# Performance work log

Measured on AMD Instinct MI355X. Metric: run time of the kernel, lower is better.

Reference implementation:

```python
import jax, jax.numpy as jnp
import numpy as np

IM_H, IM_W = 32, 32
HEADS, HEAD_DIM = 8, 32
IN_DIM = 256
OUT_DIM = 256
N = IM_H * IM_W


def _relative_indices(h, w):
    # replicate torch meshgrid('ij') + flatten logic
    gy, gx = np.meshgrid(np.arange(h), np.arange(w), indexing='ij')
    pos = np.stack([gy.reshape(-1), gx.reshape(-1)])  # (2, n)
    rel = pos[:, :, None] - pos[:, None, :]           # (2, n, n)
    r0 = (rel[0] + (h - 1)) * (2 * w - 1)
    r1 = rel[1] + (w - 1)
    return (r0 + r1).reshape(-1)                      # (n*n,)

_REL_IDX = jnp.asarray(_relative_indices(IM_H, IM_W), dtype=jnp.int32)


def setup_inputs() -> dict:
    key = jax.random.key(0)
    ks = jax.random.split(key, 8)
    d_inner = HEADS * HEAD_DIM
    x = jax.random.normal(ks[0], (16, N, IN_DIM), dtype=jnp.float32)
    Wq = jax.random.normal(ks[1], (IN_DIM, d_inner), dtype=jnp.float32) / np.sqrt(IN_DIM)
    Wk = jax.random.normal(ks[2], (IN_DIM, d_inner), dtype=jnp.float32) / np.sqrt(IN_DIM)
    Wv = jax.random.normal(ks[3], (IN_DIM, d_inner), dtype=jnp.float32) / np.sqrt(IN_DIM)
    bias_table = jax.random.normal(ks[4], ((2 * IM_H - 1) * (2 * IM_W - 1), HEADS), dtype=jnp.float32)
    Wo = jax.random.normal(ks[5], (d_inner, OUT_DIM), dtype=jnp.float32) / np.sqrt(d_inner)
    bo = jax.random.normal(ks[6], (OUT_DIM,), dtype=jnp.float32) * 0.01
    return {"x": x, "Wq": Wq, "Wk": Wk, "Wv": Wv, "bias_table": bias_table, "Wo": Wo, "bo": bo}


def reference(x, Wq, Wk, Wv, bias_table, Wo, bo):
    b, n, _ = x.shape
    scale = HEAD_DIM ** (-0.5)
    # QKV projections -> [b, h, n, d]
    def proj(W):
        return (x @ W).reshape(b, n, HEADS, HEAD_DIM).transpose(0, 2, 1, 3)
    Q, K, V = proj(Wq), proj(Wk), proj(Wv)
    # gathered relative position bias -> [1, h, n, n]
    bias = bias_table[_REL_IDX].reshape(n, n, HEADS).transpose(2, 0, 1)[None]
    scores = jnp.einsum('bhnd,bhmd->bhnm', Q, K) * scale + bias
    attn = jax.nn.softmax(scores, axis=-1)
    out = jnp.einsum('bhnm,bhmd->bhnd', attn, V)
    out = out.transpose(0, 2, 1, 3).reshape(b, n, HEADS * HEAD_DIM)
    return out @ Wo + bo  # dropout is identity in eval mode
```

## Files before the change

### kernel.cpp

```cpp
#include <hip/hip_runtime.h>


using f32x4  = __attribute__((ext_vector_type(4))) float;
using bf16x8 = __attribute__((ext_vector_type(8))) short;

__device__ __forceinline__ short f2bf(float f) {
  union { float f; unsigned u; } v; v.f = f;
  return (short)((v.u + 0x7FFFu + ((v.u >> 16) & 1u)) >> 16);
}
__device__ __forceinline__ f32x4 mfma_k32(bf16x8 a, bf16x8 b, f32x4 c) {
  return __builtin_amdgcn_mfma_f32_16x16x32_bf16(a, b, c, 0, 0, 0);
}
__device__ __forceinline__ int cvt_pk_bf16(float lo, float hi) {
  int r;
  asm("v_cvt_pk_bf16_f32 %0, %1, %2" : "=v"(r) : "v"(lo), "v"(hi));
  return r;
}

__global__ __launch_bounds__(256) void k_prep(const float* __restrict__ Wq,
    const float* __restrict__ Wk, const float* __restrict__ Wv,
    const float* __restrict__ Wo, short* __restrict__ WT,
    const float* __restrict__ bt, float* __restrict__ Tg) {
  int bx = blockIdx.x;
  if (bx < 1024) {
    int wid = bx >> 8, n = bx & 255, k = threadIdx.x;
    const float* W = wid == 0 ? Wq : wid == 1 ? Wk : wid == 2 ? Wv : Wo;
    WT[wid * 65536 + n * 256 + k] = f2bf(W[k * 256 + n]);
  } else {
    int idx = (bx - 1024) * 256 + threadIdx.x;
    int h = idx >> 12, i = idx & 4095;
    if (i < 3969) Tg[idx] = bt[i * 8 + h] * 1.4426950408889634f;
  }
}

__global__ __launch_bounds__(256) void k_qkv(const float* __restrict__ x,
    const short* __restrict__ WT,
    short* __restrict__ Q, short* __restrict__ K, short* __restrict__ Vt) {
  __shared__ short Wlds[2][4096];
  char* lbase = (char*)Wlds;
  const int tid = threadIdx.x;
  const int w = tid >> 6, l = tid & 63, lr = l & 15, lg = l >> 4;
  const int m0 = blockIdx.x * 64;
  const int wi = blockIdx.y;
  const char* Wb = (const char*)(WT + wi * 65536);
  const float* xrow = x + (size_t)(m0 + w * 16 + lr) * 256;
  bf16x8 af[8];
  #pragma unroll
  for (int kc = 0; kc < 8; ++kc) {
    float4 a = *reinterpret_cast<const float4*>(xrow + kc * 32 + lg * 8);
    float4 c = *reinterpret_cast<const float4*>(xrow + kc * 32 + lg * 8 + 4);
    union { int i4[4]; bf16x8 v; } u;
    u.i4[0] = cvt_pk_bf16(a.x, a.y);
    u.i4[1] = cvt_pk_bf16(a.z, a.w);
    u.i4[2] = cvt_pk_bf16(c.x, c.y);
    u.i4[3] = cvt_pk_bf16(c.z, c.w);
    af[kc] = u.v;
  }
  const int Lb0 = tid * 16, Lb1 = 4096 + tid * 16;
  const int P0 = Lb0 ^ (((Lb0 >> 9) & 7) << 4);
  const int P1 = Lb1 ^ (((Lb1 >> 9) & 7) << 4);
  int rdo[8];
  #pragma unroll
  for (int kc = 0; kc < 8; ++kc) {
    int Lg = lr * 512 + kc * 64 + lg * 16;
    rdo[kc] = Lg ^ ((lr & 7) << 4);
  }
  {
    int4 s0 = *reinterpret_cast<const int4*>(Wb + Lb0);
    int4 s1 = *reinterpret_cast<const int4*>(Wb + Lb1);
    *reinterpret_cast<int4*>(lbase + P0) = s0;
    *reinterpret_cast<int4*>(lbase + P1) = s1;
  }
  __syncthreads();
  #pragma unroll 2
  for (int nt = 0; nt < 16; ++nt) {
    const int cur = nt & 1, nxt = cur ^ 1;
    int4 t0, t1;
    if (nt < 15) {
      t0 = *reinterpret_cast<const int4*>(Wb + (nt + 1) * 8192 + Lb0);
      t1 = *reinterpret_cast<const int4*>(Wb + (nt + 1) * 8192 + Lb1);
    }
    f32x4 acc = {0.f, 0.f, 0.f, 0.f};
    #pragma unroll
    for (int kc = 0; kc < 8; ++kc) {
      bf16x8 bfr = *reinterpret_cast<const bf16x8*>(lbase + cur * 8192 + rdo[kc]);
      acc = mfma_k32(af[kc], bfr, acc);
    }
    int colb = nt * 16 + lr;
    int h = colb >> 5, d = colb & 31;
    if (wi == 2) {
      int m = m0 + w * 16 + lg * 4;
      int b = m >> 10, n0 = m & 1023;
      int js = n0 >> 5;
      int lgv = (n0 & 15) >> 2, hi = (n0 >> 4) & 1;
      int jp = lgv * 8 + hi * 4;
      short4 vv;
      vv.x = f2bf(acc[0]); vv.y = f2bf(acc[1]);
      vv.z = f2bf(acc[2]); vv.w = f2bf(acc[3]);
      *reinterpret_cast<short4*>(
          &Vt[(((size_t)(b * 8 + h) * 32 + js) << 10) + d * 32 + jp]) = vv;
    } else {
      #pragma unroll
      for (int r = 0; r < 4; ++r) {
        int m = m0 + w * 16 + lg * 4 + r;
        int b = m >> 10, n = m & 1023;
        short val = f2bf(acc[r]);
        if (wi == 0)
          Q[((size_t)(b * 8 + h) * 1024 + n) * 32 + d] = val;
        else
          K[((size_t)(b * 8 + h) * 1024 + n) * 32 + d] = val;
      }
    }
    if (nt < 15) {
      *reinterpret_cast<int4*>(lbase + nxt * 8192 + P0) = t0;
      *reinterpret_cast<int4*>(lbase + nxt * 8192 + P1) = t1;
    }
    __syncthreads();
  }
}

__global__ __launch_bounds__(256) void k_attn(const short* __restrict__ Q,
    const short* __restrict__ K, const short* __restrict__ Vt,
    const float* __restrict__ Tg, short* __restrict__ aout) {
  __shared__ float Tlds[3969];
  const int tid = threadIdx.x, bid = blockIdx.x;
  const int h = bid & 7, qt = (bid >> 3) & 7, b = bid >> 6;
  const float* Th = Tg + (h << 12);
  for (int t = tid; t < 3969; t += 256) Tlds[t] = Th[t];
  __syncthreads();
  const int w = tid >> 6, l = tid & 63, lr = l & 15, lg = l >> 4;
  const size_t hoff = (size_t)(b * 8 + h) << 15;
  const short* Qh = Q + hoff;
  const short* Kh = K + hoff;
  const short* Vh = Vt + hoff;
  const int ita = qt * 4 + w;
  const int i0a = ita * 16;
  const int i0b = i0a + 512;
  const int yia = ita >> 1;
  const int pbase = ((ita & 1) << 4) + lr - lg * 4 + 31;
  bf16x8 qfa = *reinterpret_cast<const bf16x8*>(&Qh[(i0a + lr) * 32 + lg * 8]);
  bf16x8 qfb = *reinterpret_cast<const bf16x8*>(&Qh[(i0b + lr) * 32 + lg * 8]);
  f32x4 oa0 = {0.f,0.f,0.f,0.f}, oa1 = {0.f,0.f,0.f,0.f};
  f32x4 ob0 = {0.f,0.f,0.f,0.f}, ob1 = {0.f,0.f,0.f,0.f};
  float lsa = 0.f, lsb = 0.f;
  const float cs = 0.17677669529663688f * 1.4426950408889634f;
  const int koff0 = lr * 32 + lg * 8, koff1 = (16 + lr) * 32 + lg * 8;
  bf16x8 kf0 = *reinterpret_cast<const bf16x8*>(&Kh[koff0]);
  bf16x8 kf1 = *reinterpret_cast<const bf16x8*>(&Kh[koff1]);
  bf16x8 vf0 = *reinterpret_cast<const bf16x8*>(&Vh[koff0]);
  bf16x8 vf1 = *reinterpret_cast<const bf16x8*>(&Vh[koff1]);
  #pragma unroll 2
  for (int js = 0; js < 32; ++js) {
    const int jn = (js + 1) & 31;
    bf16x8 nkf0 = *reinterpret_cast<const bf16x8*>(&Kh[(jn << 10) + koff0]);
    bf16x8 nkf1 = *reinterpret_cast<const bf16x8*>(&Kh[(jn << 10) + koff1]);
    bf16x8 nvf0 = *reinterpret_cast<const bf16x8*>(&Vh[(jn << 10) + koff0]);
    bf16x8 nvf1 = *reinterpret_cast<const bf16x8*>(&Vh[(jn << 10) + koff1]);
    f32x4 z = {0.f, 0.f, 0.f, 0.f};
    f32x4 sa0 = mfma_k32(kf0, qfa, z);
    f32x4 sa1 = mfma_k32(kf1, qfa, z);
    f32x4 sb0 = mfma_k32(kf0, qfb, z);
    f32x4 sb1 = mfma_k32(kf1, qfb, z);
    const float* TrowA = &Tlds[(yia - js + 31) * 63];
    const float* TrowB = TrowA + 16 * 63;
    float pa0[4], pa1[4], pb0[4], pb1[4];
    #pragma unroll
    for (int r = 0; r < 4; ++r) {
      pa0[r] = __builtin_amdgcn_exp2f(fmaf(sa0[r], cs, TrowA[pbase - r]));
      pa1[r] = __builtin_amdgcn_exp2f(fmaf(sa1[r], cs, TrowA[pbase - 16 - r]));
      pb0[r] = __builtin_amdgcn_exp2f(fmaf(sb0[r], cs, TrowB[pbase - r]));
      pb1[r] = __builtin_amdgcn_exp2f(fmaf(sb1[r], cs, TrowB[pbase - 16 - r]));
      lsa += pa0[r] + pa1[r];
      lsb += pb0[r] + pb1[r];
    }
    union { int i4[4]; bf16x8 v; } pka, pkb;
    pka.i4[0] = cvt_pk_bf16(pa0[0], pa0[1]);
    pka.i4[1] = cvt_pk_bf16(pa0[2], pa0[3]);
    pka.i4[2] = cvt_pk_bf16(pa1[0], pa1[1]);
    pka.i4[3] = cvt_pk_bf16(pa1[2], pa1[3]);
    pkb.i4[0] = cvt_pk_bf16(pb0[0], pb0[1]);
    pkb.i4[1] = cvt_pk_bf16(pb0[2], pb0[3]);
    pkb.i4[2] = cvt_pk_bf16(pb1[0], pb1[1]);
    pkb.i4[3] = cvt_pk_bf16(pb1[2], pb1[3]);
    oa0 = mfma_k32(pka.v, vf0, oa0);
    oa1 = mfma_k32(pka.v, vf1, oa1);
    ob0 = mfma_k32(pkb.v, vf0, ob0);
    ob1 = mfma_k32(pkb.v, vf1, ob1);
    kf0 = nkf0; kf1 = nkf1; vf0 = nvf0; vf1 = nvf1;
  }
  {
    float s = lsa + __shfl_xor(lsa, 16);
    s += __shfl_xor(s, 32);
    float inv = 1.0f / s;
    #pragma unroll
    for (int r = 0; r < 4; ++r) {
      float invr = __shfl(inv, lg * 4 + r);
      int n = i0a + lg * 4 + r;
      size_t base = ((size_t)b << 18) + (size_t)n * 256 + h * 32;
      aout[base + lr]      = f2bf(oa0[r] * invr);
      aout[base + 16 + lr] = f2bf(oa1[r] * invr);
    }
  }
  {
    float s = lsb + __shfl_xor(lsb, 16);
    s += __shfl_xor(s, 32);
    float inv = 1.0f / s;
    #pragma unroll
    for (int r = 0; r < 4; ++r) {
      float invr = __shfl(inv, lg * 4 + r);
      int n = i0b + lg * 4 + r;
      size_t base = ((size_t)b << 18) + (size_t)n * 256 + h * 32;
      aout[base + lr]      = f2bf(ob0[r] * invr);
      aout[base + 16 + lr] = f2bf(ob1[r] * invr);
    }
  }
}

__global__ __launch_bounds__(256) void k_outproj(const short* __restrict__ aout,
    const short* __restrict__ WoT, const float* __restrict__ bo,
    float* __restrict__ out) {
  __shared__ short Wlds[2][4096];
  char* lbase = (char*)Wlds;
  const int tid = threadIdx.x;
  const int w = tid >> 6, l = tid & 63, lr = l & 15, lg = l >> 4;
  const int m0 = blockIdx.x * 64;
  const char* Wb = (const char*)WoT;
  const short* arow = aout + (size_t)(m0 + w * 16 + lr) * 256;
  bf16x8 af[8];
  #pragma unroll
  for (int kc = 0; kc < 8; ++kc)
    af[kc] = *reinterpret_cast<const bf16x8*>(arow + kc * 32 + lg * 8);
  const int Lb0 = tid * 16, Lb1 = 4096 + tid * 16;
  const int P0 = Lb0 ^ (((Lb0 >> 9) & 7) << 4);
  const int P1 = Lb1 ^ (((Lb1 >> 9) & 7) << 4);
  int rdo[8];
  #pragma unroll
  for (int kc = 0; kc < 8; ++kc) {
    int Lg = lr * 512 + kc * 64 + lg * 16;
    rdo[kc] = Lg ^ ((lr & 7) << 4);
  }
  {
    int4 s0 = *reinterpret_cast<const int4*>(Wb + Lb0);
    int4 s1 = *reinterpret_cast<const int4*>(Wb + Lb1);
    *reinterpret_cast<int4*>(lbase + P0) = s0;
    *reinterpret_cast<int4*>(lbase + P1) = s1;
  }
  __syncthreads();
  #pragma unroll 2
  for (int nt = 0; nt < 16; ++nt) {
    const int cur = nt & 1, nxt = cur ^ 1;
    int4 t0, t1;
    if (nt < 15) {
      t0 = *reinterpret_cast<const int4*>(Wb + (nt + 1) * 8192 + Lb0);
      t1 = *reinterpret_cast<const int4*>(Wb + (nt + 1) * 8192 + Lb1);
    }
    f32x4 acc = {0.f, 0.f, 0.f, 0.f};
    #pragma unroll
    for (int kc = 0; kc < 8; ++kc) {
      bf16x8 bfr = *reinterpret_cast<const bf16x8*>(lbase + cur * 8192 + rdo[kc]);
      acc = mfma_k32(af[kc], bfr, acc);
    }
    int colb = nt * 16 + lr;
    float bias = bo[colb];
    #pragma unroll
    for (int r = 0; r < 4; ++r) {
      int m = m0 + w * 16 + lg * 4 + r;
      out[(size_t)m * 256 + colb] = acc[r] + bias;
    }
    if (nt < 15) {
      *reinterpret_cast<int4*>(lbase + nxt * 8192 + P0) = t0;
      *reinterpret_cast<int4*>(lbase + nxt * 8192 + P1) = t1;
    }
    __syncthreads();
  }
}

extern "C" void kernel_launch(void* const* d_in, const int* in_sizes, int n_in,
                              void* d_out, int out_size, void* d_ws, size_t ws_size,
                              hipStream_t stream) {
  const float* x  = (const float*)d_in[0];
  const float* Wq = (const float*)d_in[1];
  const float* Wk = (const float*)d_in[2];
  const float* Wv = (const float*)d_in[3];
  const float* bt = (const float*)d_in[4];
  const float* Wo = (const float*)d_in[5];
  const float* bo = (const float*)d_in[6];
  float* out = (float*)d_out;
  char* ws = (char*)d_ws;
  short* WT   = (short*)ws;
  short* Qs   = (short*)(ws + 512 * 1024);
  short* Ks   = Qs + 4194304;
  short* Vts  = Ks + 4194304;
  short* aout = Vts + 4194304;
  float* Tg   = (float*)(ws + 512 * 1024 + 4ull * 8388608);

  k_prep<<<1152, 256, 0, stream>>>(Wq, Wk, Wv, Wo, WT, bt, Tg);
  k_qkv<<<dim3(256, 3), 256, 0, stream>>>(x, WT, Qs, Ks, Vts);
  k_attn<<<1024, 256, 0, stream>>>(Qs, Ks, Vts, Tg, aout);
  k_outproj<<<256, 256, 0, stream>>>(aout, WT + 3 * 65536, bo, out);
}
```

Before: 80.37 us.

## Split attention key loop across two wave groups and merge via LDS

Doubles the attention block to 512 threads, with the two halves each processing 16 of the 32 key tiles for the same query rows. Partial outputs and row sums from the second half go through shared memory and are added by the first half before normalization and store. This halves the serial loop length per wave and exposes more parallel work, at the cost of extra LDS usage, a block barrier, and idle waves during the epilogue.

```diff
diff --git a/kernel.cpp b/kernel.cpp
--- a/kernel.cpp
+++ b/kernel.cpp
@@ -119,16 +119,19 @@
   }
 }
 
-__global__ __launch_bounds__(256) void k_attn(const short* __restrict__ Q,
+__global__ __launch_bounds__(512) void k_attn(const short* __restrict__ Q,
     const short* __restrict__ K, const short* __restrict__ Vt,
     const float* __restrict__ Tg, short* __restrict__ aout) {
   __shared__ float Tlds[3969];
+  __shared__ float mO[4][4][4][64];
+  __shared__ float mls[4][2][64];
   const int tid = threadIdx.x, bid = blockIdx.x;
   const int h = bid & 7, qt = (bid >> 3) & 7, b = bid >> 6;
   const float* Th = Tg + (h << 12);
-  for (int t = tid; t < 3969; t += 256) Tlds[t] = Th[t];
+  for (int t = tid; t < 3969; t += 512) Tlds[t] = Th[t];
   __syncthreads();
-  const int w = tid >> 6, l = tid & 63, lr = l & 15, lg = l >> 4;
+  const int wg = tid >> 6, l = tid & 63, lr = l & 15, lg = l >> 4;
+  const int w = wg & 3, jh = wg >> 2;
   const size_t hoff = (size_t)(b * 8 + h) << 15;
   const short* Qh = Q + hoff;
   const short* Kh = K + hoff;
@@ -145,13 +148,14 @@
   float lsa = 0.f, lsb = 0.f;
   const float cs = 0.17677669529663688f * 1.4426950408889634f;
   const int koff0 = lr * 32 + lg * 8, koff1 = (16 + lr) * 32 + lg * 8;
-  bf16x8 kf0 = *reinterpret_cast<const bf16x8*>(&Kh[koff0]);
-  bf16x8 kf1 = *reinterpret_cast<const bf16x8*>(&Kh[koff1]);
-  bf16x8 vf0 = *reinterpret_cast<const bf16x8*>(&Vh[koff0]);
-  bf16x8 vf1 = *reinterpret_cast<const bf16x8*>(&Vh[koff1]);
+  const int js0 = jh * 16, jsE = js0 + 16;
+  bf16x8 kf0 = *reinterpret_cast<const bf16x8*>(&Kh[(js0 << 10) + koff0]);
+  bf16x8 kf1 = *reinterpret_cast<const bf16x8*>(&Kh[(js0 << 10) + koff1]);
+  bf16x8 vf0 = *reinterpret_cast<const bf16x8*>(&Vh[(js0 << 10) + koff0]);
+  bf16x8 vf1 = *reinterpret_cast<const bf16x8*>(&Vh[(js0 << 10) + koff1]);
   #pragma unroll 2
-  for (int js = 0; js < 32; ++js) {
-    const int jn = (js + 1) & 31;
+  for (int js = js0; js < jsE; ++js) {
+    const int jn = (js + 1 < jsE) ? js + 1 : js;
     bf16x8 nkf0 = *reinterpret_cast<const bf16x8*>(&Kh[(jn << 10) + koff0]);
     bf16x8 nkf1 = *reinterpret_cast<const bf16x8*>(&Kh[(jn << 10) + koff1]);
     bf16x8 nvf0 = *reinterpret_cast<const bf16x8*>(&Vh[(jn << 10) + koff0]);
@@ -188,30 +192,51 @@
     ob1 = mfma_k32(pkb.v, vf1, ob1);
     kf0 = nkf0; kf1 = nkf1; vf0 = nvf0; vf1 = nvf1;
   }
-  {
-    float s = lsa + __shfl_xor(lsa, 16);
-    s += __shfl_xor(s, 32);
-    float inv = 1.0f / s;
+  if (jh == 1) {
     #pragma unroll
     for (int r = 0; r < 4; ++r) {
-      float invr = __shfl(inv, lg * 4 + r);
-      int n = i0a + lg * 4 + r;
-      size_t base = ((size_t)b << 18) + (size_t)n * 256 + h * 32;
-      aout[base + lr]      = f2bf(oa0[r] * invr);
-      aout[base + 16 + lr] = f2bf(oa1[r] * invr);
-    }
-  }
-  {
-    float s = lsb + __shfl_xor(lsb, 16);
-    s += __shfl_xor(s, 32);
-    float inv = 1.0f / s;
+      mO[w][0][r][l] = oa0[r];
+      mO[w][1][r][l] = oa1[r];
+      mO[w][2][r][l] = ob0[r];
+      mO[w][3][r][l] = ob1[r];
+    }
+    mls[w][0][l] = lsa;
+    mls[w][1][l] = lsb;
+  }
+  __syncthreads();
+  if (jh == 0) {
     #pragma unroll
     for (int r = 0; r < 4; ++r) {
-      float invr = __shfl(inv, lg * 4 + r);
-      int n = i0b + lg * 4 + r;
-      size_t base = ((size_t)b << 18) + (size_t)n * 256 + h * 32;
-      aout[base + lr]      = f2bf(ob0[r] * invr);
-      aout[base + 16 + lr] = f2bf(ob1[r] * invr);
+      oa0[r] += mO[w][0][r][l];
+      oa1[r] += mO[w][1][r][l];
+      ob0[r] += mO[w][2][r][l];
+      ob1[r] += mO[w][3][r][l];
+    }
+    lsa += mls[w][0][l];
+    lsb += mls[w][1][l];
+    {
+      float s = lsa + __shfl_xor(lsa, 16);
+      s += __shfl_xor(s, 32);
+      float inv = 1.0f / s;
+      #pragma unroll
+      for (int r = 0; r < 4; ++r) {
+        float invr = __shfl(inv, lg * 4 + r);
+        int n = i0a + lg * 4 + r;
+        size_t base = ((size_t)b << 18) + (size_t)n * 256 + h * 32;
+        aout[base + lr]      = f2bf(oa0[r] * invr);
+        aout[base + 16 + lr] = f2bf(oa1[r] * invr);
+      }
+      s = lsb + __shfl_xor(lsb, 16);
+      s += __shfl_xor(s, 32);
+      inv = 1.0f / s;
+      #pragma unroll
+      for (int r = 0; r < 4; ++r) {
+        float invr = __shfl(inv, lg * 4 + r);
+        int n = i0b + lg * 4 + r;
+        size_t base = ((size_t)b << 18) + (size_t)n * 256 + h * 32;
+        aout[base + lr]      = f2bf(ob0[r] * invr);
+        aout[base + 16 + lr] = f2bf(ob1[r] * invr);
+      }
     }
   }
 }
@@ -296,6 +321,6 @@
 
   k_prep<<<1152, 256, 0, stream>>>(Wq, Wk, Wv, Wo, WT, bt, Tg);
   k_qkv<<<dim3(256, 3), 256, 0, stream>>>(x, WT, Qs, Ks, Vts);
-  k_attn<<<1024, 256, 0, stream>>>(Qs, Ks, Vts, Tg, aout);
+  k_attn<<<1024, 512, 0, stream>>>(Qs, Ks, Vts, Tg, aout);
   k_outproj<<<256, 256, 0, stream>>>(aout, WT + 3 * 65536, bo, out);
 }
```

Result: no change. 78.96 us (-1.8%).
